# Performance work log

Hardware: AMD Instinct MI355X
Metric: run time of the kernel (lower is better)

Reference implementation:

```python
import jax, jax.numpy as jnp
import numpy as np

N, D, C = 4096, 1024, 1000
EPS = 1e-8


def _remove_diag(M):
    # faithful to torch M[off_diag_mask].view(h, h-1) via strided-reshape trick
    h = M.shape[0]
    return M.reshape(-1)[1:].reshape(h - 1, h + 1)[:, :-1].reshape(h, h - 1)


def _cosine_sim_matrix(x, y):
    # torch CosineSimilarity: x.y / max(||x||*||y||, eps)
    xn = jnp.linalg.norm(x, axis=-1, keepdims=True)
    yn = jnp.linalg.norm(y, axis=-1, keepdims=True)
    num = jnp.einsum('id,jd->ij', x, y)
    den = jnp.maximum(xn * yn.T, EPS)
    return num / den


def setup_inputs() -> dict:
    key = jax.random.key(0)
    k1, k2, k3, k4 = jax.random.split(key, 4)
    return {
        'inst_embed': jax.random.normal(k1, (N, D), dtype=jnp.float32),
        'anchor': jax.random.normal(k2, (N, D), dtype=jnp.float32),
        'cls_mask': jax.random.randint(k3, (C, N), 0, 2, dtype=jnp.int32),
        'labels': jax.random.randint(k4, (N,), 0, C, dtype=jnp.int64),
        'temperature': jnp.float32(1.0),
    }


def reference(inst_embed, anchor, cls_mask, labels, temperature):
    # augmentation=None branch of Conditional_Embedding_Contrastive_loss.forward
    sim = _cosine_sim_matrix(inst_embed, inst_embed)          # [N,N]
    instance_zone = jnp.exp(_remove_diag(sim) / temperature)  # [N,N-1]
    mask_neg = _remove_diag(cls_mask[labels].astype(instance_zone.dtype))  # [N,N-1]
    inst2inst_pos = instance_zone * mask_neg
    # elementwise cosine sim between inst_embed and anchor rows
    dot = jnp.sum(inst_embed * anchor, axis=-1)
    nrm = jnp.maximum(jnp.linalg.norm(inst_embed, axis=-1) * jnp.linalg.norm(anchor, axis=-1), EPS)
    inst2embed_pos = jnp.exp((dot / nrm) / temperature)       # [N]
    numerator = inst2inst_pos.sum(axis=1) + inst2embed_pos
    denominator = inst2embed_pos + instance_zone.sum(axis=1)
    return -jnp.mean(jnp.log(numerator / denominator))
```

## Files before the change

### kernel.cpp

```cpp
#include <hip/hip_runtime.h>
#include <hip/hip_bf16.h>
#include <math.h>


#define NN   4096
#define DD   1024
#define NCLS 1000
#define EPSF 1e-8f
#define MW   (NN / 32)
#define NTILE 528
#define SLOTS 32

typedef short bf16x8 __attribute__((ext_vector_type(8)));
typedef float f32x4  __attribute__((ext_vector_type(4)));

__global__ __launch_bounds__(256) void k_pack(const int* __restrict__ cmask,
                                              const int* __restrict__ lraw,
                                              unsigned int* __restrict__ mbits,
                                              int* __restrict__ lab) {
  const int b = blockIdx.x;
  if (b < NCLS * MW / 256) {
    const int wword = b * 256 + threadIdx.x;
    const int* src = cmask + (size_t)wword * 32;
    unsigned int v = 0;
    #pragma unroll
    for (int q = 0; q < 8; ++q) {
      const int4 c = *(const int4*)(src + q * 4);
      v |= (c.x != 0 ? 1u : 0u) << (q * 4 + 0);
      v |= (c.y != 0 ? 1u : 0u) << (q * 4 + 1);
      v |= (c.z != 0 ? 1u : 0u) << (q * 4 + 2);
      v |= (c.w != 0 ? 1u : 0u) << (q * 4 + 3);
    }
    mbits[wword] = v;
  } else {
    __shared__ int stride_s;
    if (threadIdx.x == 0) {
      int stride = 2;
      #pragma unroll
      for (int t = 0; t < 8; ++t) {
        int lo = lraw[2 * t], hi = lraw[2 * t + 1];
        if (hi != 0 || (unsigned)lo >= (unsigned)NCLS) { stride = 1; break; }
      }
      stride_s = stride;
    }
    __syncthreads();
    const int i = (b - NCLS * MW / 256) * 256 + threadIdx.x;
    lab[i] = lraw[i * stride_s];
  }
}

__global__ __launch_bounds__(256) void k_rowstats(
    const float* __restrict__ X, const float* __restrict__ A,
    const float* __restrict__ Tp, ushort* __restrict__ Xb,
    float* __restrict__ rnx, float* __restrict__ rnT,
    float* __restrict__ epos, float* __restrict__ out) {
  const int i = blockIdx.x;
  const int t = threadIdx.x;
  const size_t base = (size_t)i * DD + t * 4;
  const float4 xv = *(const float4*)(X + base);
  const float4 av = *(const float4*)(A + base);
  float sxx = xv.x * xv.x + xv.y * xv.y + xv.z * xv.z + xv.w * xv.w;
  float saa = av.x * av.x + av.y * av.y + av.z * av.z + av.w * av.w;
  float sxa = xv.x * av.x + xv.y * av.y + xv.z * av.z + xv.w * av.w;

  ushort4 pk;
  { __hip_bfloat16 b;
    b = __float2bfloat16(xv.x); pk.x = *(const ushort*)&b;
    b = __float2bfloat16(xv.y); pk.y = *(const ushort*)&b;
    b = __float2bfloat16(xv.z); pk.z = *(const ushort*)&b;
    b = __float2bfloat16(xv.w); pk.w = *(const ushort*)&b; }
  *(ushort4*)(Xb + base) = pk;

  #pragma unroll
  for (int off = 32; off > 0; off >>= 1) {
    sxx += __shfl_down(sxx, off);
    saa += __shfl_down(saa, off);
    sxa += __shfl_down(sxa, off);
  }
  __shared__ float red[3][4];
  const int w = t >> 6;
  if ((t & 63) == 0) { red[0][w] = sxx; red[1][w] = saa; red[2][w] = sxa; }
  __syncthreads();
  if (t == 0) {
    const float a  = red[0][0] + red[0][1] + red[0][2] + red[0][3];
    const float bb = red[1][0] + red[1][1] + red[1][2] + red[1][3];
    const float c  = red[2][0] + red[2][1] + red[2][2] + red[2][3];
    const float nxi = sqrtf(a), nai = sqrtf(bb);
    const float rT  = 1.0f / Tp[0];
    const float r   = 1.0f / fmaxf(nxi, 1e-20f);
    rnx[i] = r;
    rnT[i] = r * rT;
    epos[i] = expf((c / fmaxf(nxi * nai, EPSF)) * rT);
    if (i == 0) out[0] = 0.f;
  }
}

#define BM 128
#define BK 128

__global__ __launch_bounds__(512, 4) void k_gram(
    const ushort* __restrict__ Xb, const float* __restrict__ rnx,
    const float* __restrict__ rnT,
    const int* __restrict__ lab, const unsigned int* __restrict__ mbits,
    float* __restrict__ scrF, float* __restrict__ scrM) {
  __shared__ __align__(16) char LDS[4 * BM * 64 * 2];
  char* As0 = LDS;
  char* As1 = LDS + 16384;
  char* Bs0 = LDS + 32768;
  char* Bs1 = LDS + 49152;
  const int tid  = threadIdx.x;
  const int lane = tid & 63;
  const int w    = tid >> 6;
  const int wr   = w >> 2;
  const int wc   = w & 3;

  const int xcd = blockIdx.x & 7;
  const int l   = blockIdx.x >> 3;
  const int p   = (xcd << 1) + (l >= 33);
  const int q   = (l >= 33) ? (l - 33) : l;
  int by, bx;
  if (q < 32 - p) { by = p;      bx = p + q; }
  else            { by = 31 - p; bx = 31 - p + (q - (32 - p)); }
  const bool offdiag = (bx != by);
  const int i0 = by * BM;
  const int j0 = bx * BM;

  const int sslot = (lane & 7) ^ (lane >> 3);

  f32x4 acc[4][2];
  #pragma unroll
  for (int m = 0; m < 4; ++m)
    #pragma unroll
    for (int n = 0; n < 2; ++n)
      acc[m][n] = (f32x4){0.f, 0.f, 0.f, 0.f};

  const ushort* pA[2];
  const ushort* pB[2];
  #pragma unroll
  for (int q2 = 0; q2 < 2; ++q2) {
    const int row = (w << 4) + (q2 << 3) + (lane >> 3);
    pA[q2] = Xb + (size_t)(i0 + row) * DD + sslot * 8;
    pB[q2] = Xb + (size_t)(j0 + row) * DD + sslot * 8;
  }

  for (int k0 = 0; k0 < DD; k0 += BK) {
    #pragma unroll
    for (int q2 = 0; q2 < 2; ++q2) {
      const int ldo = ((w << 1) + q2) * 1024;
      __builtin_amdgcn_global_load_lds(
          (const __attribute__((address_space(1))) void*)(pA[q2] + k0),
          (__attribute__((address_space(3))) void*)(As0 + ldo), 16, 0, 0);
      __builtin_amdgcn_global_load_lds(
          (const __attribute__((address_space(1))) void*)(pA[q2] + k0 + 64),
          (__attribute__((address_space(3))) void*)(As1 + ldo), 16, 0, 0);
      __builtin_amdgcn_global_load_lds(
          (const __attribute__((address_space(1))) void*)(pB[q2] + k0),
          (__attribute__((address_space(3))) void*)(Bs0 + ldo), 16, 0, 0);
      __builtin_amdgcn_global_load_lds(
          (const __attribute__((address_space(1))) void*)(pB[q2] + k0 + 64),
          (__attribute__((address_space(3))) void*)(Bs1 + ldo), 16, 0, 0);
    }
    __syncthreads();

    #pragma unroll
    for (int kh = 0; kh < 2; ++kh) {
      const char* Ab = kh ? As1 : As0;
      const char* Bb = kh ? Bs1 : Bs0;
      #pragma unroll
      for (int ks = 0; ks < 2; ++ks) {
        const int slot = ((ks << 2) + (lane >> 4)) ^ (lane & 7);
        bf16x8 af[4], bfr[2];
        #pragma unroll
        for (int m = 0; m < 4; ++m) {
          const int r = (wr << 6) + (m << 4) + (lane & 15);
          af[m] = *(const bf16x8*)(Ab + r * 128 + (slot << 4));
        }
        #pragma unroll
        for (int n = 0; n < 2; ++n) {
          const int r = (wc << 5) + (n << 4) + (lane & 15);
          bfr[n] = *(const bf16x8*)(Bb + r * 128 + (slot << 4));
        }
        #pragma unroll
        for (int m = 0; m < 4; ++m)
          #pragma unroll
          for (int n = 0; n < 2; ++n)
            acc[m][n] = __builtin_amdgcn_mfma_f32_16x16x32_bf16(af[m], bfr[n], acc[m][n], 0, 0, 0);
      }
    }
    __syncthreads();
  }

  float* LF = (float*)LDS;
  float* LM = LF + 512;
  float* GF = LM + 512;
  float* GM = GF + 256;

  float rnT_j[2];
  unsigned long long wj[2];
  #pragma unroll
  for (int n = 0; n < 2; ++n) {
    const int j = j0 + (wc << 5) + (n << 4) + (lane & 15);
    rnT_j[n] = rnT[j];
    wj[n] = *(const unsigned long long*)(mbits + (size_t)lab[j] * MW + (i0 >> 5) + (wr << 1));
  }
  float pse[2] = {0.f, 0.f}, psm[2] = {0.f, 0.f};

  #pragma unroll
  for (int m = 0; m < 4; ++m) {
    #pragma unroll
    for (int r = 0; r < 4; ++r) {
      const int irow = (m << 4) + ((lane >> 4) << 2) + r;
      const int i = i0 + (wr << 6) + irow;
      const float rni = rnx[i];
      const unsigned int wi = mbits[(size_t)lab[i] * MW + (j0 >> 5) + wc];
      float se = 0.f, sm = 0.f;
      #pragma unroll
      for (int n = 0; n < 2; ++n) {
        const int j = j0 + (wc << 5) + (n << 4) + (lane & 15);
        float e = __expf(acc[m][n][r] * rni * rnT_j[n]);
        if (i == j) e = 0.f;
        se += e;
        const int bposj = (n << 4) + (lane & 15);
        sm += ((wi >> bposj) & 1u) ? e : 0.f;
        pse[n] += e;
        psm[n] += ((wj[n] >> irow) & 1ull) ? e : 0.f;
      }
      #pragma unroll
      for (int off = 1; off < 16; off <<= 1) {
        se += __shfl_xor(se, off);
        sm += __shfl_xor(sm, off);
      }
      if ((lane & 15) == 0) {
        LF[(wc << 7) + (wr << 6) + irow] = se;
        LM[(wc << 7) + (wr << 6) + irow] = sm;
      }
    }
  }
  if (offdiag) {
    #pragma unroll
    for (int n = 0; n < 2; ++n) {
      float se = pse[n], sm = psm[n];
      se += __shfl_xor(se, 16); se += __shfl_xor(se, 32);
      sm += __shfl_xor(sm, 16); sm += __shfl_xor(sm, 32);
      if (lane < 16) {
        GF[(wr << 7) + (wc << 5) + (n << 4) + lane] = se;
        GM[(wr << 7) + (wc << 5) + (n << 4) + lane] = sm;
      }
    }
  }
  __syncthreads();

  if (tid < 128) {
    scrF[(size_t)bx * NN + i0 + tid] = LF[tid] + LF[128 + tid] + LF[256 + tid] + LF[384 + tid];
    if (offdiag) scrF[(size_t)by * NN + j0 + tid] = GF[tid] + GF[128 + tid];
  } else if (tid < 256) {
    const int u = tid - 128;
    scrM[(size_t)bx * NN + i0 + u] = LM[u] + LM[128 + u] + LM[256 + u] + LM[384 + u];
    if (offdiag) scrM[(size_t)by * NN + j0 + u] = GM[u] + GM[128 + u];
  }
}

__global__ __launch_bounds__(256) void k_final(
    const float* __restrict__ scrF, const float* __restrict__ scrM,
    const float* __restrict__ epos, float* __restrict__ out) {
  const int idx = blockIdx.x * 256 + threadIdx.x;
  float sf = 0.f, sm = 0.f;
  #pragma unroll
  for (int s = 0; s < SLOTS; ++s) {
    sf += scrF[(size_t)s * NN + idx];
    sm += scrM[(size_t)s * NN + idx];
  }
  const float ep  = epos[idx];
  const float num = sm + ep;
  const float den = ep + sf;
  float v = (logf(den) - logf(num)) * (1.0f / (float)NN);
  #pragma unroll
  for (int off = 32; off > 0; off >>= 1) v += __shfl_down(v, off);
  __shared__ float red[4];
  if ((threadIdx.x & 63) == 0) red[threadIdx.x >> 6] = v;
  __syncthreads();
  if (threadIdx.x == 0) atomicAdd(out, red[0] + red[1] + red[2] + red[3]);
}

extern "C" void kernel_launch(void* const* d_in, const int* in_sizes, int n_in,
                              void* d_out, int out_size, void* d_ws, size_t ws_size,
                              hipStream_t stream) {
  const float* X     = (const float*)d_in[0];
  const float* A     = (const float*)d_in[1];
  const int*   cmask = (const int*)d_in[2];
  const int*   lraw  = (const int*)d_in[3];
  const float* Tp    = (const float*)d_in[4];
  float* out = (float*)d_out;

  char* ws = (char*)d_ws;
  ushort* Xb   = (ushort*)ws;
  float* rnx   = (float*)(ws + (size_t)NN * DD * 2);
  float* rnT   = rnx + NN;
  float* epos  = rnT + NN;
  int*   lab   = (int*)(epos + NN);
  unsigned int* mbits = (unsigned int*)(lab + NN);
  float* scrF  = (float*)(mbits + (size_t)NCLS * MW);
  float* scrM  = scrF + (size_t)SLOTS * NN;

  hipLaunchKernelGGL(k_pack,     dim3(NCLS * MW / 256 + NN / 256), dim3(256), 0, stream, cmask, lraw, mbits, lab);
  hipLaunchKernelGGL(k_rowstats, dim3(NN),     dim3(256), 0, stream, X, A, Tp, Xb, rnx, rnT, epos, out);
  hipLaunchKernelGGL(k_gram,     dim3(NTILE),  dim3(512), 0, stream, Xb, rnx, rnT, lab, mbits, scrF, scrM);
  hipLaunchKernelGGL(k_final,    dim3(NN/256), dim3(256), 0, stream, scrF, scrM, epos, out);
}
```

Before: 79.53 us.

## Split each gram tile into two half-row blocks and double scratch slots

```diff
diff --git a/kernel.cpp b/kernel.cpp
--- a/kernel.cpp
+++ b/kernel.cpp
@@ -9,7 +9,8 @@
 #define EPSF 1e-8f
 #define MW   (NN / 32)
 #define NTILE 528
-#define SLOTS 32
+#define NBLK  1056
+#define SLOTS 64
 
 typedef short bf16x8 __attribute__((ext_vector_type(8)));
 typedef float f32x4  __attribute__((ext_vector_type(4)));
@@ -17,7 +18,8 @@
 __global__ __launch_bounds__(256) void k_pack(const int* __restrict__ cmask,
                                               const int* __restrict__ lraw,
                                               unsigned int* __restrict__ mbits,
-                                              int* __restrict__ lab) {
+                                              int* __restrict__ lab,
+                                              float4* __restrict__ scrz) {
   const int b = blockIdx.x;
   if (b < NCLS * MW / 256) {
     const int wword = b * 256 + threadIdx.x;
@@ -32,7 +34,7 @@
       v |= (c.w != 0 ? 1u : 0u) << (q * 4 + 3);
     }
     mbits[wword] = v;
-  } else {
+  } else if (b < NCLS * MW / 256 + NN / 256) {
     __shared__ int stride_s;
     if (threadIdx.x == 0) {
       int stride = 2;
@@ -46,6 +48,9 @@
     __syncthreads();
     const int i = (b - NCLS * MW / 256) * 256 + threadIdx.x;
     lab[i] = lraw[i * stride_s];
+  } else {
+    const int zb = b - (NCLS * MW / 256 + NN / 256);
+    scrz[(size_t)zb * 256 + threadIdx.x] = (float4){0.f, 0.f, 0.f, 0.f};
   }
 }
 
@@ -95,35 +100,31 @@
   }
 }
 
-#define BM 128
-#define BK 128
-
-__global__ __launch_bounds__(512, 4) void k_gram(
+#define BK 64
+
+__global__ __launch_bounds__(256, 4) void k_gram(
     const ushort* __restrict__ Xb, const float* __restrict__ rnx,
     const float* __restrict__ rnT,
     const int* __restrict__ lab, const unsigned int* __restrict__ mbits,
     float* __restrict__ scrF, float* __restrict__ scrM) {
-  __shared__ __align__(16) char LDS[4 * BM * 64 * 2];
-  char* As0 = LDS;
-  char* As1 = LDS + 16384;
-  char* Bs0 = LDS + 32768;
-  char* Bs1 = LDS + 49152;
+  __shared__ __align__(16) char As[64 * 128];
+  __shared__ __align__(16) char Bs[128 * 128];
   const int tid  = threadIdx.x;
   const int lane = tid & 63;
   const int w    = tid >> 6;
-  const int wr   = w >> 2;
-  const int wc   = w & 3;
-
-  const int xcd = blockIdx.x & 7;
-  const int l   = blockIdx.x >> 3;
-  const int p   = (xcd << 1) + (l >= 33);
-  const int q   = (l >= 33) ? (l - 33) : l;
+
+  const int h    = blockIdx.x & 1;
+  const int tile = blockIdx.x >> 1;
+  const int xcd  = tile & 7;
+  const int l    = tile >> 3;
+  const int p    = (xcd << 1) + (l >= 33);
+  const int q    = (l >= 33) ? (l - 33) : l;
   int by, bx;
   if (q < 32 - p) { by = p;      bx = p + q; }
   else            { by = 31 - p; bx = 31 - p + (q - (32 - p)); }
   const bool offdiag = (bx != by);
-  const int i0 = by * BM;
-  const int j0 = bx * BM;
+  const int i0h = by * 128 + h * 64;
+  const int j0  = bx * 128;
 
   const int sslot = (lane & 7) ^ (lane >> 3);
 
@@ -135,73 +136,62 @@
       acc[m][n] = (f32x4){0.f, 0.f, 0.f, 0.f};
 
   const ushort* pA[2];
-  const ushort* pB[2];
-  #pragma unroll
-  for (int q2 = 0; q2 < 2; ++q2) {
-    const int row = (w << 4) + (q2 << 3) + (lane >> 3);
-    pA[q2] = Xb + (size_t)(i0 + row) * DD + sslot * 8;
-    pB[q2] = Xb + (size_t)(j0 + row) * DD + sslot * 8;
-  }
+  const ushort* pB[4];
+  #pragma unroll
+  for (int q2 = 0; q2 < 2; ++q2)
+    pA[q2] = Xb + (size_t)(i0h + (w << 4) + (q2 << 3) + (lane >> 3)) * DD + sslot * 8;
+  #pragma unroll
+  for (int q2 = 0; q2 < 4; ++q2)
+    pB[q2] = Xb + (size_t)(j0 + (w << 5) + (q2 << 3) + (lane >> 3)) * DD + sslot * 8;
 
   for (int k0 = 0; k0 < DD; k0 += BK) {
     #pragma unroll
-    for (int q2 = 0; q2 < 2; ++q2) {
-      const int ldo = ((w << 1) + q2) * 1024;
+    for (int q2 = 0; q2 < 2; ++q2)
       __builtin_amdgcn_global_load_lds(
           (const __attribute__((address_space(1))) void*)(pA[q2] + k0),
-          (__attribute__((address_space(3))) void*)(As0 + ldo), 16, 0, 0);
-      __builtin_amdgcn_global_load_lds(
-          (const __attribute__((address_space(1))) void*)(pA[q2] + k0 + 64),
-          (__attribute__((address_space(3))) void*)(As1 + ldo), 16, 0, 0);
+          (__attribute__((address_space(3))) void*)(As + ((w << 1) + q2) * 1024), 16, 0, 0);
+    #pragma unroll
+    for (int q2 = 0; q2 < 4; ++q2)
       __builtin_amdgcn_global_load_lds(
           (const __attribute__((address_space(1))) void*)(pB[q2] + k0),
-          (__attribute__((address_space(3))) void*)(Bs0 + ldo), 16, 0, 0);
-      __builtin_amdgcn_global_load_lds(
-          (const __attribute__((address_space(1))) void*)(pB[q2] + k0 + 64),
-          (__attribute__((address_space(3))) void*)(Bs1 + ldo), 16, 0, 0);
-    }
+          (__attribute__((address_space(3))) void*)(Bs + ((w << 2) + q2) * 1024), 16, 0, 0);
     __syncthreads();
 
     #pragma unroll
-    for (int kh = 0; kh < 2; ++kh) {
-      const char* Ab = kh ? As1 : As0;
-      const char* Bb = kh ? Bs1 : Bs0;
-      #pragma unroll
-      for (int ks = 0; ks < 2; ++ks) {
-        const int slot = ((ks << 2) + (lane >> 4)) ^ (lane & 7);
-        bf16x8 af[4], bfr[2];
+    for (int ks = 0; ks < 2; ++ks) {
+      const int slot = ((ks << 2) + (lane >> 4)) ^ (lane & 7);
+      bf16x8 af[4], bfr[2];
+      #pragma unroll
+      for (int m = 0; m < 4; ++m) {
+        const int r = (m << 4) + (lane & 15);
+        af[m] = *(const bf16x8*)(As + r * 128 + (slot << 4));
+      }
+      #pragma unroll
+      for (int n = 0; n < 2; ++n) {
+        const int r = (w << 5) + (n << 4) + (lane & 15);
+        bfr[n] = *(const bf16x8*)(Bs + r * 128 + (slot << 4));
+      }
+      #pragma unroll
+      for (int m = 0; m < 4; ++m)
         #pragma unroll
-        for (int m = 0; m < 4; ++m) {
-          const int r = (wr << 6) + (m << 4) + (lane & 15);
-          af[m] = *(const bf16x8*)(Ab + r * 128 + (slot << 4));
-        }
-        #pragma unroll
-        for (int n = 0; n < 2; ++n) {
-          const int r = (wc << 5) + (n << 4) + (lane & 15);
-          bfr[n] = *(const bf16x8*)(Bb + r * 128 + (slot << 4));
-        }
-        #pragma unroll
-        for (int m = 0; m < 4; ++m)
-          #pragma unroll
-          for (int n = 0; n < 2; ++n)
-            acc[m][n] = __builtin_amdgcn_mfma_f32_16x16x32_bf16(af[m], bfr[n], acc[m][n], 0, 0, 0);
-      }
+        for (int n = 0; n < 2; ++n)
+          acc[m][n] = __builtin_amdgcn_mfma_f32_16x16x32_bf16(af[m], bfr[n], acc[m][n], 0, 0, 0);
     }
     __syncthreads();
   }
 
-  float* LF = (float*)LDS;
-  float* LM = LF + 512;
-  float* GF = LM + 512;
-  float* GM = GF + 256;
+  float* LF = (float*)As;
+  float* LM = LF + 256;
+  float* GF = LM + 256;
+  float* GM = GF + 128;
 
   float rnT_j[2];
   unsigned long long wj[2];
   #pragma unroll
   for (int n = 0; n < 2; ++n) {
-    const int j = j0 + (wc << 5) + (n << 4) + (lane & 15);
+    const int j = j0 + (w << 5) + (n << 4) + (lane & 15);
     rnT_j[n] = rnT[j];
-    wj[n] = *(const unsigned long long*)(mbits + (size_t)lab[j] * MW + (i0 >> 5) + (wr << 1));
+    wj[n] = *(const unsigned long long*)(mbits + (size_t)lab[j] * MW + (i0h >> 5));
   }
   float pse[2] = {0.f, 0.f}, psm[2] = {0.f, 0.f};
 
@@ -210,13 +200,13 @@
     #pragma unroll
     for (int r = 0; r < 4; ++r) {
       const int irow = (m << 4) + ((lane >> 4) << 2) + r;
-      const int i = i0 + (wr << 6) + irow;
+      const int i = i0h + irow;
       const float rni = rnx[i];
-      const unsigned int wi = mbits[(size_t)lab[i] * MW + (j0 >> 5) + wc];
+      const unsigned int wi = mbits[(size_t)lab[i] * MW + (j0 >> 5) + w];
       float se = 0.f, sm = 0.f;
       #pragma unroll
       for (int n = 0; n < 2; ++n) {
-        const int j = j0 + (wc << 5) + (n << 4) + (lane & 15);
+        const int j = j0 + (w << 5) + (n << 4) + (lane & 15);
         float e = __expf(acc[m][n][r] * rni * rnT_j[n]);
         if (i == j) e = 0.f;
         se += e;
@@ -231,8 +221,8 @@
         sm += __shfl_xor(sm, off);
       }
       if ((lane & 15) == 0) {
-        LF[(wc << 7) + (wr << 6) + irow] = se;
-        LM[(wc << 7) + (wr << 6) + irow] = sm;
+        LF[(w << 6) + irow] = se;
+        LM[(w << 6) + irow] = sm;
       }
     }
   }
@@ -243,20 +233,24 @@
       se += __shfl_xor(se, 16); se += __shfl_xor(se, 32);
       sm += __shfl_xor(sm, 16); sm += __shfl_xor(sm, 32);
       if (lane < 16) {
-        GF[(wr << 7) + (wc << 5) + (n << 4) + lane] = se;
-        GM[(wr << 7) + (wc << 5) + (n << 4) + lane] = sm;
+        GF[(w << 5) + (n << 4) + lane] = se;
+        GM[(w << 5) + (n << 4) + lane] = sm;
       }
     }
   }
   __syncthreads();
 
-  if (tid < 128) {
-    scrF[(size_t)bx * NN + i0 + tid] = LF[tid] + LF[128 + tid] + LF[256 + tid] + LF[384 + tid];
-    if (offdiag) scrF[(size_t)by * NN + j0 + tid] = GF[tid] + GF[128 + tid];
-  } else if (tid < 256) {
+  if (tid < 64) {
+    scrF[(size_t)(h * 32 + bx) * NN + i0h + tid] =
+        LF[tid] + LF[64 + tid] + LF[128 + tid] + LF[192 + tid];
+  } else if (tid < 128) {
+    const int u = tid - 64;
+    scrM[(size_t)(h * 32 + bx) * NN + i0h + u] =
+        LM[u] + LM[64 + u] + LM[128 + u] + LM[192 + u];
+  } else if (offdiag) {
     const int u = tid - 128;
-    scrM[(size_t)bx * NN + i0 + u] = LM[u] + LM[128 + u] + LM[256 + u] + LM[384 + u];
-    if (offdiag) scrM[(size_t)by * NN + j0 + u] = GM[u] + GM[128 + u];
+    scrF[(size_t)(h * 32 + by) * NN + j0 + u] = GF[u];
+    scrM[(size_t)(h * 32 + by) * NN + j0 + u] = GM[u];
   }
 }
 
@@ -302,8 +296,10 @@
   float* scrF  = (float*)(mbits + (size_t)NCLS * MW);
   float* scrM  = scrF + (size_t)SLOTS * NN;
 
-  hipLaunchKernelGGL(k_pack,     dim3(NCLS * MW / 256 + NN / 256), dim3(256), 0, stream, cmask, lraw, mbits, lab);
+  const int packg = NCLS * MW / 256 + NN / 256 + 1024;
+
+  hipLaunchKernelGGL(k_pack,     dim3(packg),  dim3(256), 0, stream, cmask, lraw, mbits, lab, (float4*)scrF);
   hipLaunchKernelGGL(k_rowstats, dim3(NN),     dim3(256), 0, stream, X, A, Tp, Xb, rnx, rnT, epos, out);
-  hipLaunchKernelGGL(k_gram,     dim3(NTILE),  dim3(512), 0, stream, Xb, rnx, rnT, lab, mbits, scrF, scrM);
+  hipLaunchKernelGGL(k_gram,     dim3(NBLK),   dim3(256), 0, stream, Xb, rnx, rnT, lab, mbits, scrF, scrM);
   hipLaunchKernelGGL(k_final,    dim3(NN/256), dim3(256), 0, stream, scrF, scrM, epos, out);
 }
```

New measurement: 89.64 us. 12.7% more time.

## Double-buffer Gram K-loop with async LDS prefetch of next tile

Applied to the files above, without the earlier changes.

```diff
diff --git a/kernel.cpp b/kernel.cpp
--- a/kernel.cpp
+++ b/kernel.cpp
@@ -96,18 +96,15 @@
 }
 
 #define BM 128
-#define BK 128
+#define BK 64
+#define NSTEP (DD / BK)
 
 __global__ __launch_bounds__(512, 4) void k_gram(
     const ushort* __restrict__ Xb, const float* __restrict__ rnx,
     const float* __restrict__ rnT,
     const int* __restrict__ lab, const unsigned int* __restrict__ mbits,
     float* __restrict__ scrF, float* __restrict__ scrM) {
-  __shared__ __align__(16) char LDS[4 * BM * 64 * 2];
-  char* As0 = LDS;
-  char* As1 = LDS + 16384;
-  char* Bs0 = LDS + 32768;
-  char* Bs1 = LDS + 49152;
+  __shared__ __align__(16) char LDS[2 * 2 * BM * 64 * 2];
   const int tid  = threadIdx.x;
   const int lane = tid & 63;
   const int w    = tid >> 6;
@@ -143,51 +140,56 @@
     pB[q2] = Xb + (size_t)(j0 + row) * DD + sslot * 8;
   }
 
-  for (int k0 = 0; k0 < DD; k0 += BK) {
-    #pragma unroll
-    for (int q2 = 0; q2 < 2; ++q2) {
-      const int ldo = ((w << 1) + q2) * 1024;
-      __builtin_amdgcn_global_load_lds(
-          (const __attribute__((address_space(1))) void*)(pA[q2] + k0),
-          (__attribute__((address_space(3))) void*)(As0 + ldo), 16, 0, 0);
-      __builtin_amdgcn_global_load_lds(
-          (const __attribute__((address_space(1))) void*)(pA[q2] + k0 + 64),
-          (__attribute__((address_space(3))) void*)(As1 + ldo), 16, 0, 0);
-      __builtin_amdgcn_global_load_lds(
-          (const __attribute__((address_space(1))) void*)(pB[q2] + k0),
-          (__attribute__((address_space(3))) void*)(Bs0 + ldo), 16, 0, 0);
-      __builtin_amdgcn_global_load_lds(
-          (const __attribute__((address_space(1))) void*)(pB[q2] + k0 + 64),
-          (__attribute__((address_space(3))) void*)(Bs1 + ldo), 16, 0, 0);
-    }
-    __syncthreads();
-
-    #pragma unroll
-    for (int kh = 0; kh < 2; ++kh) {
-      const char* Ab = kh ? As1 : As0;
-      const char* Bb = kh ? Bs1 : Bs0;
-      #pragma unroll
-      for (int ks = 0; ks < 2; ++ks) {
-        const int slot = ((ks << 2) + (lane >> 4)) ^ (lane & 7);
-        bf16x8 af[4], bfr[2];
+  #define STAGE(BUF, K0)                                                        \
+    {                                                                           \
+      char* Ad = LDS + (BUF) * 32768;                                           \
+      char* Bd = Ad + 16384;                                                    \
+      _Pragma("unroll")                                                         \
+      for (int q2 = 0; q2 < 2; ++q2) {                                          \
+        const int ldo = ((w << 1) + q2) * 1024;                                 \
+        __builtin_amdgcn_global_load_lds(                                       \
+            (const __attribute__((address_space(1))) void*)(pA[q2] + (K0)),     \
+            (__attribute__((address_space(3))) void*)(Ad + ldo), 16, 0, 0);     \
+        __builtin_amdgcn_global_load_lds(                                       \
+            (const __attribute__((address_space(1))) void*)(pB[q2] + (K0)),     \
+            (__attribute__((address_space(3))) void*)(Bd + ldo), 16, 0, 0);     \
+      }                                                                         \
+    }
+
+  STAGE(0, 0)
+
+  for (int s = 0; s < NSTEP; ++s) {
+    const int cur = s & 1;
+    if (s + 1 < NSTEP) {
+      STAGE(cur ^ 1, (s + 1) * BK)
+      asm volatile("s_waitcnt vmcnt(4)\n\ts_barrier" ::: "memory");
+    } else {
+      asm volatile("s_waitcnt vmcnt(0)\n\ts_barrier" ::: "memory");
+    }
+
+    const char* Ab = LDS + cur * 32768;
+    const char* Bb = Ab + 16384;
+    #pragma unroll
+    for (int ks = 0; ks < 2; ++ks) {
+      const int slot = ((ks << 2) + (lane >> 4)) ^ (lane & 7);
+      bf16x8 af[4], bfr[2];
+      #pragma unroll
+      for (int m = 0; m < 4; ++m) {
+        const int r = (wr << 6) + (m << 4) + (lane & 15);
+        af[m] = *(const bf16x8*)(Ab + r * 128 + (slot << 4));
+      }
+      #pragma unroll
+      for (int n = 0; n < 2; ++n) {
+        const int r = (wc << 5) + (n << 4) + (lane & 15);
+        bfr[n] = *(const bf16x8*)(Bb + r * 128 + (slot << 4));
+      }
+      #pragma unroll
+      for (int m = 0; m < 4; ++m)
         #pragma unroll
-        for (int m = 0; m < 4; ++m) {
-          const int r = (wr << 6) + (m << 4) + (lane & 15);
-          af[m] = *(const bf16x8*)(Ab + r * 128 + (slot << 4));
-        }
-        #pragma unroll
-        for (int n = 0; n < 2; ++n) {
-          const int r = (wc << 5) + (n << 4) + (lane & 15);
-          bfr[n] = *(const bf16x8*)(Bb + r * 128 + (slot << 4));
-        }
-        #pragma unroll
-        for (int m = 0; m < 4; ++m)
-          #pragma unroll
-          for (int n = 0; n < 2; ++n)
-            acc[m][n] = __builtin_amdgcn_mfma_f32_16x16x32_bf16(af[m], bfr[n], acc[m][n], 0, 0, 0);
-      }
-    }
-    __syncthreads();
+        for (int n = 0; n < 2; ++n)
+          acc[m][n] = __builtin_amdgcn_mfma_f32_16x16x32_bf16(af[m], bfr[n], acc[m][n], 0, 0, 0);
+    }
+    asm volatile("s_barrier" ::: "memory");
   }
 
   float* LF = (float*)LDS;
```

New measurement: 78.90 us. About the same (-0.8%).

## Pipeline gram K-loop with 4-stage LDS ring and async global-to-LDS prefetch

Applied to the files above, without the earlier changes.

```diff
diff --git a/kernel.cpp b/kernel.cpp
--- a/kernel.cpp
+++ b/kernel.cpp
@@ -10,6 +10,7 @@
 #define MW   (NN / 32)
 #define NTILE 528
 #define SLOTS 32
+#define NSTEP 32
 
 typedef short bf16x8 __attribute__((ext_vector_type(8)));
 typedef float f32x4  __attribute__((ext_vector_type(4)));
@@ -96,18 +97,13 @@
 }
 
 #define BM 128
-#define BK 128
 
 __global__ __launch_bounds__(512, 4) void k_gram(
     const ushort* __restrict__ Xb, const float* __restrict__ rnx,
     const float* __restrict__ rnT,
     const int* __restrict__ lab, const unsigned int* __restrict__ mbits,
     float* __restrict__ scrF, float* __restrict__ scrM) {
-  __shared__ __align__(16) char LDS[4 * BM * 64 * 2];
-  char* As0 = LDS;
-  char* As1 = LDS + 16384;
-  char* Bs0 = LDS + 32768;
-  char* Bs1 = LDS + 49152;
+  __shared__ __align__(16) char LDS[4 * 16384];
   const int tid  = threadIdx.x;
   const int lane = tid & 63;
   const int w    = tid >> 6;
@@ -125,7 +121,9 @@
   const int i0 = by * BM;
   const int j0 = bx * BM;
 
-  const int sslot = (lane & 7) ^ (lane >> 3);
+  const int qs = (lane & 3) ^ ((lane >> 3) & 3);
+  const ushort* gA = Xb + (size_t)(i0 + (w << 4) + (lane >> 2)) * DD + qs * 8;
+  const ushort* gB = Xb + (size_t)(j0 + (w << 4) + (lane >> 2)) * DD + qs * 8;
 
   f32x4 acc[4][2];
   #pragma unroll
@@ -134,61 +132,66 @@
     for (int n = 0; n < 2; ++n)
       acc[m][n] = (f32x4){0.f, 0.f, 0.f, 0.f};
 
-  const ushort* pA[2];
-  const ushort* pB[2];
-  #pragma unroll
-  for (int q2 = 0; q2 < 2; ++q2) {
-    const int row = (w << 4) + (q2 << 3) + (lane >> 3);
-    pA[q2] = Xb + (size_t)(i0 + row) * DD + sslot * 8;
-    pB[q2] = Xb + (size_t)(j0 + row) * DD + sslot * 8;
-  }
-
-  for (int k0 = 0; k0 < DD; k0 += BK) {
-    #pragma unroll
-    for (int q2 = 0; q2 < 2; ++q2) {
-      const int ldo = ((w << 1) + q2) * 1024;
-      __builtin_amdgcn_global_load_lds(
-          (const __attribute__((address_space(1))) void*)(pA[q2] + k0),
-          (__attribute__((address_space(3))) void*)(As0 + ldo), 16, 0, 0);
-      __builtin_amdgcn_global_load_lds(
-          (const __attribute__((address_space(1))) void*)(pA[q2] + k0 + 64),
-          (__attribute__((address_space(3))) void*)(As1 + ldo), 16, 0, 0);
-      __builtin_amdgcn_global_load_lds(
-          (const __attribute__((address_space(1))) void*)(pB[q2] + k0),
-          (__attribute__((address_space(3))) void*)(Bs0 + ldo), 16, 0, 0);
-      __builtin_amdgcn_global_load_lds(
-          (const __attribute__((address_space(1))) void*)(pB[q2] + k0 + 64),
-          (__attribute__((address_space(3))) void*)(Bs1 + ldo), 16, 0, 0);
-    }
-    __syncthreads();
-
-    #pragma unroll
-    for (int kh = 0; kh < 2; ++kh) {
-      const char* Ab = kh ? As1 : As0;
-      const char* Bb = kh ? Bs1 : Bs0;
-      #pragma unroll
-      for (int ks = 0; ks < 2; ++ks) {
-        const int slot = ((ks << 2) + (lane >> 4)) ^ (lane & 7);
-        bf16x8 af[4], bfr[2];
-        #pragma unroll
-        for (int m = 0; m < 4; ++m) {
-          const int r = (wr << 6) + (m << 4) + (lane & 15);
-          af[m] = *(const bf16x8*)(Ab + r * 128 + (slot << 4));
-        }
-        #pragma unroll
-        for (int n = 0; n < 2; ++n) {
-          const int r = (wc << 5) + (n << 4) + (lane & 15);
-          bfr[n] = *(const bf16x8*)(Bb + r * 128 + (slot << 4));
-        }
-        #pragma unroll
-        for (int m = 0; m < 4; ++m)
-          #pragma unroll
-          for (int n = 0; n < 2; ++n)
-            acc[m][n] = __builtin_amdgcn_mfma_f32_16x16x32_bf16(af[m], bfr[n], acc[m][n], 0, 0, 0);
-      }
-    }
-    __syncthreads();
-  }
+  #define STAGE(T)                                                             \
+    {                                                                          \
+      char* bp = LDS + ((T) & 3) * 16384;                                      \
+      __builtin_amdgcn_global_load_lds(                                        \
+          (const __attribute__((address_space(1))) void*)(gA + (T) * 32),      \
+          (__attribute__((address_space(3))) void*)(bp + w * 1024), 16, 0, 0); \
+      __builtin_amdgcn_global_load_lds(                                        \
+          (const __attribute__((address_space(1))) void*)(gB + (T) * 32),      \
+          (__attribute__((address_space(3))) void*)(bp + 8192 + w * 1024), 16, 0, 0); \
+    }
+
+  const int rph = ((lane & 15) >> 1) & 3;
+  int aoff[4], boff[2];
+  #pragma unroll
+  for (int m = 0; m < 4; ++m) {
+    const int r = (wr << 6) + (m << 4) + (lane & 15);
+    aoff[m] = r * 64 + (((lane >> 4) ^ rph) << 4);
+  }
+  #pragma unroll
+  for (int n = 0; n < 2; ++n) {
+    const int r = (wc << 5) + (n << 4) + (lane & 15);
+    boff[n] = 8192 + r * 64 + (((lane >> 4) ^ rph) << 4);
+  }
+
+  STAGE(0) STAGE(1) STAGE(2)
+
+  for (int t = 0; t <= NSTEP - 4; ++t) {
+    STAGE(t + 3)
+    asm volatile("s_waitcnt vmcnt(6)\n\ts_barrier" ::: "memory");
+    const char* bp = LDS + (t & 3) * 16384;
+    bf16x8 af[4], bfr[2];
+    #pragma unroll
+    for (int m = 0; m < 4; ++m) af[m] = *(const bf16x8*)(bp + aoff[m]);
+    #pragma unroll
+    for (int n = 0; n < 2; ++n) bfr[n] = *(const bf16x8*)(bp + boff[n]);
+    __builtin_amdgcn_s_setprio(1);
+    #pragma unroll
+    for (int m = 0; m < 4; ++m)
+      #pragma unroll
+      for (int n = 0; n < 2; ++n)
+        acc[m][n] = __builtin_amdgcn_mfma_f32_16x16x32_bf16(af[m], bfr[n], acc[m][n], 0, 0, 0);
+    __builtin_amdgcn_s_setprio(0);
+    asm volatile("s_barrier" ::: "memory");
+  }
+  asm volatile("s_waitcnt vmcnt(0)\n\ts_barrier" ::: "memory");
+  #pragma unroll
+  for (int t = NSTEP - 3; t < NSTEP; ++t) {
+    const char* bp = LDS + (t & 3) * 16384;
+    bf16x8 af[4], bfr[2];
+    #pragma unroll
+    for (int m = 0; m < 4; ++m) af[m] = *(const bf16x8*)(bp + aoff[m]);
+    #pragma unroll
+    for (int n = 0; n < 2; ++n) bfr[n] = *(const bf16x8*)(bp + boff[n]);
+    #pragma unroll
+    for (int m = 0; m < 4; ++m)
+      #pragma unroll
+      for (int n = 0; n < 2; ++n)
+        acc[m][n] = __builtin_amdgcn_mfma_f32_16x16x32_bf16(af[m], bfr[n], acc[m][n], 0, 0, 0);
+  }
+  __syncthreads();
 
   float* LF = (float*)LDS;
   float* LM = LF + 512;
```

Measured after the change: 77.09 us. 1.03x faster.
